# Optimization experiments

Hardware: AMD Instinct MI355X
Metric: run time of the kernel (lower is better)

## Reference

```python
import jax, jax.numpy as jnp
import numpy as np

NUM_TEAMS = 100000
INPUT_SIZE = 128
HIDDEN = 128
NUM_MATCHES = 1000000
OUT = 3


def setup_inputs() -> dict:
    key = jax.random.key(0)
    ks = jax.random.split(key, 10)
    s_ih = 1.0 / np.sqrt(HIDDEN)
    inputs = jax.random.normal(ks[0], (NUM_TEAMS, INPUT_SIZE), dtype=jnp.float32)
    hx = jax.random.normal(ks[1], (NUM_TEAMS, HIDDEN), dtype=jnp.float32)
    cx = jax.random.normal(ks[2], (NUM_TEAMS, HIDDEN), dtype=jnp.float32)
    matches = jax.random.randint(ks[3], (NUM_MATCHES, 2), 0, NUM_TEAMS, dtype=jnp.int64)
    W_ih = jax.random.uniform(ks[4], (4 * HIDDEN, INPUT_SIZE), jnp.float32, -s_ih, s_ih)
    W_hh = jax.random.uniform(ks[5], (4 * HIDDEN, HIDDEN), jnp.float32, -s_ih, s_ih)
    b_ih = jax.random.uniform(ks[6], (4 * HIDDEN,), jnp.float32, -s_ih, s_ih)
    b_hh = jax.random.uniform(ks[7], (4 * HIDDEN,), jnp.float32, -s_ih, s_ih)
    s_o = 1.0 / np.sqrt(2 * HIDDEN)
    W_out = jax.random.uniform(ks[8], (OUT, 2 * HIDDEN), jnp.float32, -s_o, s_o)
    b_out = jax.random.uniform(ks[9], (OUT,), jnp.float32, -s_o, s_o)
    return {"inputs": inputs, "hx": hx, "cx": cx, "matches": matches,
            "W_ih": W_ih, "W_hh": W_hh, "b_ih": b_ih, "b_hh": b_hh,
            "W_out": W_out, "b_out": b_out}


def reference(inputs, hx, cx, matches, W_ih, W_hh, b_ih, b_hh, W_out, b_out):
    # Batched LSTMCell step across all teams (replaces per-team Python loop).
    gates = inputs @ W_ih.T + b_ih + hx @ W_hh.T + b_hh  # [T, 4H]
    i_g, f_g, g_g, o_g = jnp.split(gates, 4, axis=1)
    c_new = jax.nn.sigmoid(f_g) * cx + jax.nn.sigmoid(i_g) * jnp.tanh(g_g)
    h_new = jax.nn.sigmoid(o_g) * jnp.tanh(c_new)  # [T, H]
    # Fused gather + concat + linear + softmax for all matches.
    home = h_new[matches[:, 0]]  # [M, H]
    away = h_new[matches[:, 1]]  # [M, H]
    feat = jnp.concatenate([home, away], axis=1)  # [M, 2H]
    logits = feat @ W_out.T + b_out  # [M, 3]
    pmf = jax.nn.softmax(logits, axis=-1)
    return pmf
```

## Files before the change

### kernel.cpp

```cpp
#include <hip/hip_runtime.h>
#include <hip/hip_bf16.h>

typedef __bf16 bf16x8 __attribute__((ext_vector_type(8)));
typedef float f32x4 __attribute__((ext_vector_type(4)));

#define NUM_TEAMS 100000
#define NUM_MATCHES 1000000
#define LOG2E 1.4426950408889634f
#define NWG 3126
#define XQ 390
#define XR 6

__device__ __forceinline__ unsigned short f2bf(float x) {
    __hip_bfloat16 h = __float2bfloat16(x);
    return reinterpret_cast<unsigned short&>(h);
}
__device__ __forceinline__ unsigned int cvtpk(float a, float b) {
    unsigned int r;
    asm("v_cvt_pk_bf16_f32 %0, %1, %2" : "=v"(r) : "v"(a), "v"(b));
    return r;
}
__device__ __forceinline__ float exp2_(float x) {
    float r; asm("v_exp_f32 %0, %1" : "=v"(r) : "v"(x)); return r;
}
__device__ __forceinline__ float rcp_(float x) {
    float r; asm("v_rcp_f32 %0, %1" : "=v"(r) : "v"(x)); return r;
}

__global__ __launch_bounds__(256) void prep_kernel(
    const float* __restrict__ W_ih, const float* __restrict__ W_hh,
    const float* __restrict__ b_ih, const float* __restrict__ b_hh,
    unsigned short* __restrict__ Wpk, float* __restrict__ biasc)
{
    int gid = blockIdx.x * 256 + threadIdx.x;
    int e = gid & 7;
    int chunk = gid >> 3;
    int l15 = chunk & 15;
    int l4 = (chunk >> 4) & 3;
    int rest = chunk >> 6;
    int ks = rest & 7;
    int gate = (rest >> 3) & 3;
    int G = rest >> 5;
    int row = gate * 128 + G * 16 + l15;
    int k = ks * 32 + l4 * 8 + e;
    float v = (k < 128) ? W_ih[row * 128 + k] : W_hh[row * 128 + (k - 128)];
    Wpk[gid] = f2bf(v);
    if (gid < 512) {
        float b = b_ih[gid] + b_hh[gid];
        float scale = ((gid >> 7) == 2) ? (2.0f * LOG2E) : (-LOG2E);
        biasc[gid] = b * scale;
    }
}

__global__ __launch_bounds__(256, 4) void lstm_kernel(
    const float* __restrict__ inputs, const float* __restrict__ hx,
    const float* __restrict__ cx, const unsigned short* __restrict__ Wpk,
    const float* __restrict__ biasc, const float* __restrict__ W_out,
    float* __restrict__ projP)
{
    __shared__ __align__(16) unsigned short Abf[64 * 256];
    __shared__ float Wlds[768];
    const int tid = threadIdx.x;

    const int orig = blockIdx.x;
    const int xcd = orig & 7, idx = orig >> 3;
    const int wgid = (xcd < XR ? xcd * (XQ + 1) : XR * (XQ + 1) + (xcd - XR) * XQ) + idx;
    const int tile = wgid >> 1, ch = wgid & 1;
    const int brow = tile * 64;

    const int lane = tid & 63;
    const int w = tid >> 6;
    const int l15 = lane & 15, l4 = lane >> 4;
    const int hl = w * 16 + l15;
    const int hcol = ch * 64 + hl;

    {
        const int r0 = tid >> 4, seg = tid & 15;
        #pragma unroll
        for (int p = 0; p < 4; ++p) {
            int r = p * 16 + r0;
            int team = brow + r; if (team >= NUM_TEAMS) team = NUM_TEAMS - 1;
            const float* src = (seg < 8) ? inputs + (size_t)team * 128 + seg * 16
                                         : hx + (size_t)team * 128 + (seg - 8) * 16;
            float4 v0 = *reinterpret_cast<const float4*>(src);
            float4 v1 = *reinterpret_cast<const float4*>(src + 4);
            float4 v2 = *reinterpret_cast<const float4*>(src + 8);
            float4 v3 = *reinterpret_cast<const float4*>(src + 12);
            char* lbw = reinterpret_cast<char*>(Abf);
            int base = r * 512 + seg * 32;
            int swz = (r & 7) << 4;
            uint4 q0, q1;
            q0.x = cvtpk(v0.x, v0.y); q0.y = cvtpk(v0.z, v0.w);
            q0.z = cvtpk(v1.x, v1.y); q0.w = cvtpk(v1.z, v1.w);
            q1.x = cvtpk(v2.x, v2.y); q1.y = cvtpk(v2.z, v2.w);
            q1.z = cvtpk(v3.x, v3.y); q1.w = cvtpk(v3.z, v3.w);
            *reinterpret_cast<uint4*>(lbw + (base ^ swz)) = q0;
            *reinterpret_cast<uint4*>(lbw + ((base + 16) ^ swz)) = q1;
        }
        Wlds[tid] = W_out[tid];
        Wlds[256 + tid] = W_out[256 + tid];
        Wlds[512 + tid] = W_out[512 + tid];
    }

    const unsigned short* bpg = Wpk + (size_t)(ch * 4 + w) * 16384 + lane * 8;
    const float bic = biasc[hcol];
    const float bfc = biasc[128 + hcol];
    const float bgc = biasc[256 + hcol];
    const float boc = biasc[384 + hcol];
    const int swzA = (l15 & 7) << 4;
    const int kf = l4 * 16;
    const char* pArow = reinterpret_cast<const char*>(Abf) + l15 * 512;

    f32x4 acc[4][4] = {};

    __syncthreads();

    #pragma unroll
    for (int ks = 0; ks < 8; ++ks) {
        bf16x8 b0 = *(const bf16x8*)(bpg + ks * 512);
        bf16x8 b1 = *(const bf16x8*)(bpg + 4096 + ks * 512);
        bf16x8 b2 = *(const bf16x8*)(bpg + 8192 + ks * 512);
        bf16x8 b3 = *(const bf16x8*)(bpg + 12288 + ks * 512);
        const int ko = (ks * 64 + kf) ^ swzA;
        #pragma unroll
        for (int m = 0; m < 4; ++m) {
            bf16x8 af = *(const bf16x8*)(pArow + m * 8192 + ko);
            acc[m][0] = __builtin_amdgcn_mfma_f32_16x16x32_bf16(af, b0, acc[m][0], 0, 0, 0);
            acc[m][1] = __builtin_amdgcn_mfma_f32_16x16x32_bf16(af, b1, acc[m][1], 0, 0, 0);
            acc[m][2] = __builtin_amdgcn_mfma_f32_16x16x32_bf16(af, b2, acc[m][2], 0, 0, 0);
            acc[m][3] = __builtin_amdgcn_mfma_f32_16x16x32_bf16(af, b3, acc[m][3], 0, 0, 0);
        }
    }

    float cxa[16];
    #pragma unroll
    for (int m = 0; m < 4; ++m)
        #pragma unroll
        for (int j = 0; j < 4; ++j) {
            int team = brow + m * 16 + l4 * 4 + j;
            if (team >= NUM_TEAMS) team = NUM_TEAMS - 1;
            cxa[m * 4 + j] = cx[(size_t)team * 128 + hcol];
        }

    __syncthreads();

    {
        char* lb = reinterpret_cast<char*>(Abf);
        #pragma unroll
        for (int m = 0; m < 4; ++m) {
            #pragma unroll
            for (int j = 0; j < 4; ++j) {
                float si = rcp_(1.0f + exp2_(fmaf(acc[m][0][j], -LOG2E, bic)));
                float sf = rcp_(1.0f + exp2_(fmaf(acc[m][1][j], -LOG2E, bfc)));
                float tg = fmaf(-2.0f, rcp_(1.0f + exp2_(fmaf(acc[m][2][j], 2.0f * LOG2E, bgc))), 1.0f);
                float so = rcp_(1.0f + exp2_(fmaf(acc[m][3][j], -LOG2E, boc)));
                float cn = fmaf(sf, cxa[m * 4 + j], si * tg);
                float tc = fmaf(-2.0f, rcp_(1.0f + exp2_(cn * (2.0f * LOG2E))), 1.0f);
                float hn = so * tc;
                int t = m * 16 + l4 * 4 + j;
                *reinterpret_cast<float*>(lb + ((t * 256 + hl * 4) ^ ((t & 7) << 4))) = hn;
            }
        }
    }
    __syncthreads();

    {
        int tl = tid >> 2, sub = tid & 3;
        const char* lb = reinterpret_cast<const char*>(Abf);
        int hbase = tl * 256 + sub * 64;
        int hswz = (tl & 7) << 4;
        float a0 = 0.f, a1 = 0.f, a2 = 0.f, a3 = 0.f, a4 = 0.f, a5 = 0.f;
        #pragma unroll
        for (int c = 0; c < 4; ++c) {
            f32x4 h4 = *reinterpret_cast<const f32x4*>(lb + ((hbase + c * 16) ^ hswz));
            #pragma unroll
            for (int i = 0; i < 4; ++i) {
                float h = h4[i];
                int col = ch * 64 + sub * 16 + c * 4 + i;
                a0 += h * Wlds[col];       a1 += h * Wlds[256 + col]; a2 += h * Wlds[512 + col];
                a3 += h * Wlds[128 + col]; a4 += h * Wlds[384 + col]; a5 += h * Wlds[640 + col];
            }
        }
        a0 += __shfl_xor(a0, 1); a1 += __shfl_xor(a1, 1); a2 += __shfl_xor(a2, 1);
        a3 += __shfl_xor(a3, 1); a4 += __shfl_xor(a4, 1); a5 += __shfl_xor(a5, 1);
        a0 += __shfl_xor(a0, 2); a1 += __shfl_xor(a1, 2); a2 += __shfl_xor(a2, 2);
        a3 += __shfl_xor(a3, 2); a4 += __shfl_xor(a4, 2); a5 += __shfl_xor(a5, 2);
        int team = brow + tl;
        if (sub == 0 && team < NUM_TEAMS) {
            float4* o = reinterpret_cast<float4*>(projP + (size_t)team * 16 + ch * 8);
            o[0] = make_float4(a0, a1, a2, a2);
            o[1] = make_float4(a3, a4, a5, a5);
        }
    }
}

__global__ __launch_bounds__(256) void match_kernel(
    const int* __restrict__ matches, const float* __restrict__ projP,
    const float* __restrict__ b_out, float* __restrict__ out)
{
    int m = blockIdx.x * 256 + threadIdx.x;
    if (m >= NUM_MATCHES) return;
    int2 mi = reinterpret_cast<const int2*>(matches)[m];
    const float4* pp = reinterpret_cast<const float4*>(projP);
    float4 h0 = pp[(size_t)mi.x * 4 + 0];
    float4 h1 = pp[(size_t)mi.x * 4 + 2];
    float4 a0 = pp[(size_t)mi.y * 4 + 1];
    float4 a1 = pp[(size_t)mi.y * 4 + 3];
    float l0 = h0.x + h1.x + a0.x + a1.x + b_out[0];
    float l1 = h0.y + h1.y + a0.y + a1.y + b_out[1];
    float l2 = h0.z + h1.z + a0.z + a1.z + b_out[2];
    float mx = fmaxf(l0, fmaxf(l1, l2));
    float e0 = __expf(l0 - mx), e1 = __expf(l1 - mx), e2 = __expf(l2 - mx);
    float inv = 1.0f / (e0 + e1 + e2);
    out[3 * m + 0] = e0 * inv;
    out[3 * m + 1] = e1 * inv;
    out[3 * m + 2] = e2 * inv;
}

extern "C" void kernel_launch(void* const* d_in, const int* in_sizes, int n_in,
                              void* d_out, int out_size, void* d_ws, size_t ws_size,
                              hipStream_t stream) {
    const float* inputs = (const float*)d_in[0];
    const float* hx     = (const float*)d_in[1];
    const float* cx     = (const float*)d_in[2];
    const int*   matches= (const int*)d_in[3];
    const float* W_ih   = (const float*)d_in[4];
    const float* W_hh   = (const float*)d_in[5];
    const float* b_ih   = (const float*)d_in[6];
    const float* b_hh   = (const float*)d_in[7];
    const float* W_out  = (const float*)d_in[8];
    const float* b_out  = (const float*)d_in[9];
    float* out = (float*)d_out;

    char* ws = (char*)d_ws;
    unsigned short* Wpk  = (unsigned short*)ws;
    float* biasc         = (float*)(ws + 262144);
    float* projP         = (float*)(ws + (1 << 20));

    prep_kernel <<<512, 256, 0, stream>>>(W_ih, W_hh, b_ih, b_hh, Wpk, biasc);
    lstm_kernel <<<NWG, 256, 0, stream>>>(inputs, hx, cx, Wpk, biasc, W_out, projP);
    match_kernel<<<(NUM_MATCHES + 255) / 256, 256, 0, stream>>>(matches, projP, b_out, out);
}
```

Measured before the change: 77.26 us.

## Stage match outputs in LDS for float4 stores and prefetch first B fragments

After: 74.79 us. -3.2%, faster.

```diff
diff --git a/kernel.cpp b/kernel.cpp
--- a/kernel.cpp
+++ b/kernel.cpp
@@ -113,15 +113,16 @@
 
     f32x4 acc[4][4] = {};
 
-    __syncthreads();
-
-    #pragma unroll
-    for (int ks = 0; ks < 8; ++ks) {
-        bf16x8 b0 = *(const bf16x8*)(bpg + ks * 512);
-        bf16x8 b1 = *(const bf16x8*)(bpg + 4096 + ks * 512);
-        bf16x8 b2 = *(const bf16x8*)(bpg + 8192 + ks * 512);
-        bf16x8 b3 = *(const bf16x8*)(bpg + 12288 + ks * 512);
-        const int ko = (ks * 64 + kf) ^ swzA;
+    bf16x8 b0 = *(const bf16x8*)(bpg);
+    bf16x8 b1 = *(const bf16x8*)(bpg + 4096);
+    bf16x8 b2 = *(const bf16x8*)(bpg + 8192);
+    bf16x8 b3 = *(const bf16x8*)(bpg + 12288);
+
+    __syncthreads();
+
+    __builtin_amdgcn_s_setprio(1);
+    {
+        const int ko = kf ^ swzA;
         #pragma unroll
         for (int m = 0; m < 4; ++m) {
             bf16x8 af = *(const bf16x8*)(pArow + m * 8192 + ko);
@@ -131,6 +132,23 @@
             acc[m][3] = __builtin_amdgcn_mfma_f32_16x16x32_bf16(af, b3, acc[m][3], 0, 0, 0);
         }
     }
+    #pragma unroll
+    for (int ks = 1; ks < 8; ++ks) {
+        b0 = *(const bf16x8*)(bpg + ks * 512);
+        b1 = *(const bf16x8*)(bpg + 4096 + ks * 512);
+        b2 = *(const bf16x8*)(bpg + 8192 + ks * 512);
+        b3 = *(const bf16x8*)(bpg + 12288 + ks * 512);
+        const int ko = (ks * 64 + kf) ^ swzA;
+        #pragma unroll
+        for (int m = 0; m < 4; ++m) {
+            bf16x8 af = *(const bf16x8*)(pArow + m * 8192 + ko);
+            acc[m][0] = __builtin_amdgcn_mfma_f32_16x16x32_bf16(af, b0, acc[m][0], 0, 0, 0);
+            acc[m][1] = __builtin_amdgcn_mfma_f32_16x16x32_bf16(af, b1, acc[m][1], 0, 0, 0);
+            acc[m][2] = __builtin_amdgcn_mfma_f32_16x16x32_bf16(af, b2, acc[m][2], 0, 0, 0);
+            acc[m][3] = __builtin_amdgcn_mfma_f32_16x16x32_bf16(af, b3, acc[m][3], 0, 0, 0);
+        }
+    }
+    __builtin_amdgcn_s_setprio(0);
 
     float cxa[16];
     #pragma unroll
@@ -198,9 +216,11 @@
     const int* __restrict__ matches, const float* __restrict__ projP,
     const float* __restrict__ b_out, float* __restrict__ out)
 {
-    int m = blockIdx.x * 256 + threadIdx.x;
-    if (m >= NUM_MATCHES) return;
-    int2 mi = reinterpret_cast<const int2*>(matches)[m];
+    __shared__ __align__(16) float ol[768];
+    const int t = threadIdx.x;
+    int m = blockIdx.x * 256 + t;
+    int mm = (m < NUM_MATCHES) ? m : NUM_MATCHES - 1;
+    int2 mi = reinterpret_cast<const int2*>(matches)[mm];
     const float4* pp = reinterpret_cast<const float4*>(projP);
     float4 h0 = pp[(size_t)mi.x * 4 + 0];
     float4 h1 = pp[(size_t)mi.x * 4 + 2];
@@ -212,9 +232,15 @@
     float mx = fmaxf(l0, fmaxf(l1, l2));
     float e0 = __expf(l0 - mx), e1 = __expf(l1 - mx), e2 = __expf(l2 - mx);
     float inv = 1.0f / (e0 + e1 + e2);
-    out[3 * m + 0] = e0 * inv;
-    out[3 * m + 1] = e1 * inv;
-    out[3 * m + 2] = e2 * inv;
+    ol[t * 3 + 0] = e0 * inv;
+    ol[t * 3 + 1] = e1 * inv;
+    ol[t * 3 + 2] = e2 * inv;
+    __syncthreads();
+    if (t < 192) {
+        size_t fi = (size_t)blockIdx.x * 192 + t;
+        if (fi < 750000)
+            reinterpret_cast<float4*>(out)[fi] = reinterpret_cast<const float4*>(ol)[t];
+    }
 }
 
 extern "C" void kernel_launch(void* const* d_in, const int* in_sizes, int n_in,
```
